# Kernel tuning notes

Measured on AMD Instinct MI355X. Metric: run time of the kernel, lower is better.

The kernel has to match this reference:

```python
import jax, jax.numpy as jnp
import numpy as np

B, N, IN_DIM, L = 4, 512, 256, 128


def setup_inputs() -> dict:
    key = jax.random.key(0)
    k1, k2, k3, k4 = jax.random.split(key, 4)
    x = jax.random.normal(k1, (B, N, IN_DIM), dtype=jnp.float32)
    adj = jnp.ones((B, N, N), dtype=jnp.float32)
    box_num = jax.random.randint(k2, (B, 1), 0, N)  # (B,1) int
    # learned params
    W = jax.random.normal(k3, (L, IN_DIM), dtype=jnp.float32) * 0.05  # projection (no bias)
    a = jax.random.uniform(k4, (L,), dtype=jnp.float32)  # adjacency vector, U(0,1)
    return {"x": x, "adj": adj, "box_num": box_num, "W": W, "a": a}


def reference(x, adj, box_num, W, a):
    Bn, Nn, _ = x.shape
    x_hat = jnp.einsum('bnd,ld->bnl', x, W)  # (B,N,L)
    # dynamic mask: -1 where either node is padding, 0 otherwise (B,N,N)
    valid = jnp.arange(Nn)[None, :] < box_num  # (B,N) bool
    pair = valid[:, None, :] & valid[:, :, None]  # (B,N,N)
    mask = jnp.where(pair, 0.0, -1.0).astype(x.dtype)
    # (|x_i - x_j| + mask) . a  ==  |x_i - x_j| . a  +  mask * sum(a)
    diff = jnp.abs(x_hat[:, :, None, :] - x_hat[:, None, :, :])  # (B,N,N,L) big intermediate
    dist = jnp.einsum('bijd,d->bij', diff, a) + mask * jnp.sum(a)
    out = jax.nn.leaky_relu(dist)  # negative_slope 0.01 matches torch default
    out = out - jnp.max(out, axis=-1, keepdims=True)
    soft = adj * jnp.exp(out)
    soft = soft / jnp.sum(soft, axis=-1, keepdims=True) + 1e-10
    return soft
```

## Files before the change

### kernel.cpp

```cpp
#include <hip/hip_runtime.h>
#include <math.h>

namespace {

constexpr int B_ = 4;
constexpr int N_ = 512;
constexpr int D_ = 256;
constexpr int L_ = 128;
constexpr int TI = 4;

__global__ __launch_bounds__(128) void proj_kernel(
    const float* __restrict__ x, const float* __restrict__ W,
    const float* __restrict__ a, float* __restrict__ xs) {
  const int tid = threadIdx.x;
  const int b = blockIdx.z;
  const int n = blockIdx.y * 128 + tid;
  const int l0 = blockIdx.x * 4;
  const float4* __restrict__ x4 =
      reinterpret_cast<const float4*>(x + (size_t)(b * N_ + n) * D_);
  const float4* __restrict__ W4 = reinterpret_cast<const float4*>(W);
  float acc0 = 0.f, acc1 = 0.f, acc2 = 0.f, acc3 = 0.f;
#pragma unroll 4
  for (int d4 = 0; d4 < D_ / 4; ++d4) {
    const float4 xv = x4[d4];
    const float4 w0 = W4[(l0 + 0) * (D_ / 4) + d4];
    const float4 w1 = W4[(l0 + 1) * (D_ / 4) + d4];
    const float4 w2 = W4[(l0 + 2) * (D_ / 4) + d4];
    const float4 w3 = W4[(l0 + 3) * (D_ / 4) + d4];
    acc0 += xv.x * w0.x + xv.y * w0.y + xv.z * w0.z + xv.w * w0.w;
    acc1 += xv.x * w1.x + xv.y * w1.y + xv.z * w1.z + xv.w * w1.w;
    acc2 += xv.x * w2.x + xv.y * w2.y + xv.z * w2.z + xv.w * w2.w;
    acc3 += xv.x * w3.x + xv.y * w3.y + xv.z * w3.z + xv.w * w3.w;
  }
  float* o = xs + (size_t)(b * L_ + l0) * N_ + n;
  o[0 * N_] = acc0 * a[l0 + 0];
  o[1 * N_] = acc1 * a[l0 + 1];
  o[2 * N_] = acc2 * a[l0 + 2];
  o[3 * N_] = acc3 * a[l0 + 3];
}

__global__ __launch_bounds__(512) void dist_softmax_kernel(
    const float* __restrict__ xs, const float* __restrict__ adj,
    const int* __restrict__ box_num, const float* __restrict__ a,
    float* __restrict__ out) {
  const int t = threadIdx.x;
  const int j = t;
  const int i0 = blockIdx.x * TI;
  const int b = blockIdx.y;
  const int bn = box_num[b];
  const float* __restrict__ xs_b = xs + (size_t)b * L_ * N_;

  __shared__ float xi_l[L_ * TI];
  __shared__ float red[8][TI];
  __shared__ float sa_l[2];
  __shared__ float rmax_s[TI];
  __shared__ float rsinv_s[TI];

  xi_l[t] = xs_b[(t >> 2) * N_ + i0 + (t & 3)];

  {
    float sa = (t < L_) ? a[t] : 0.f;
#pragma unroll
    for (int off = 1; off < 64; off <<= 1) sa += __shfl_xor(sa, off);
    if (t == 0) sa_l[0] = sa;
    if (t == 64) sa_l[1] = sa;
  }
  __syncthreads();
  const float sum_a = sa_l[0] + sa_l[1];

  float acc[TI];
#pragma unroll
  for (int r = 0; r < TI; ++r) acc[r] = 0.f;

  const float4* __restrict__ xi4 = reinterpret_cast<const float4*>(xi_l);
#pragma unroll 4
  for (int l = 0; l < L_; ++l) {
    const float xj = xs_b[l * N_ + j];
    const float4 xi = xi4[l];
    acc[0] += fabsf(xi.x - xj);
    acc[1] += fabsf(xi.y - xj);
    acc[2] += fabsf(xi.z - xj);
    acc[3] += fabsf(xi.w - xj);
  }

  const bool vj = j < bn;
  float val[TI];
#pragma unroll
  for (int r = 0; r < TI; ++r) {
    const bool vi = (i0 + r) < bn;
    const float d = acc[r] - ((vi && vj) ? 0.f : sum_a);
    val[r] = d >= 0.f ? d : 0.01f * d;
  }

  const int lane = t & 63;
  const int wid = t >> 6;

  {
    float wm[TI];
#pragma unroll
    for (int r = 0; r < TI; ++r) {
      float m = val[r];
#pragma unroll
      for (int off = 1; off < 64; off <<= 1) m = fmaxf(m, __shfl_xor(m, off));
      wm[r] = m;
    }
    if (lane == 0) {
#pragma unroll
      for (int r = 0; r < TI; ++r) red[wid][r] = wm[r];
    }
  }
  __syncthreads();
  if (t < TI) {
    float m = red[0][t];
#pragma unroll
    for (int w = 1; w < 8; ++w) m = fmaxf(m, red[w][t]);
    rmax_s[t] = m;
  }
  __syncthreads();

  float e[TI];
  const float* __restrict__ adjp = adj + ((size_t)(b * N_ + i0)) * N_ + j;
#pragma unroll
  for (int r = 0; r < TI; ++r) {
    e[r] = adjp[(size_t)r * N_] * expf(val[r] - rmax_s[r]);
  }

  {
    float wsum[TI];
#pragma unroll
    for (int r = 0; r < TI; ++r) {
      float s = e[r];
#pragma unroll
      for (int off = 1; off < 64; off <<= 1) s += __shfl_xor(s, off);
      wsum[r] = s;
    }
    if (lane == 0) {
#pragma unroll
      for (int r = 0; r < TI; ++r) red[wid][r] = wsum[r];
    }
  }
  __syncthreads();
  if (t < TI) {
    float s = red[0][t];
#pragma unroll
    for (int w = 1; w < 8; ++w) s += red[w][t];
    rsinv_s[t] = 1.0f / s;
  }
  __syncthreads();

  float* __restrict__ op = out + ((size_t)(b * N_ + i0)) * N_ + j;
#pragma unroll
  for (int r = 0; r < TI; ++r) {
    op[(size_t)r * N_] = e[r] * rsinv_s[r] + 1e-10f;
  }
}

}

extern "C" void kernel_launch(void* const* d_in, const int* in_sizes, int n_in,
                              void* d_out, int out_size, void* d_ws,
                              size_t ws_size, hipStream_t stream) {
  const float* x = (const float*)d_in[0];
  const float* adj = (const float*)d_in[1];
  const int* box_num = (const int*)d_in[2];
  const float* W = (const float*)d_in[3];
  const float* a = (const float*)d_in[4];
  float* out = (float*)d_out;
  float* xs = (float*)d_ws;

  dim3 g1(L_ / 4, N_ / 128, B_);
  proj_kernel<<<g1, 128, 0, stream>>>(x, W, a, xs);

  dim3 g2(N_ / TI, B_);
  dist_softmax_kernel<<<g2, 512, 0, stream>>>(xs, adj, box_num, a, out);
}
```

Baseline: 29.87 us.

## Stage x tiles in LDS for projection and double rows per softmax block

```diff
diff --git a/kernel.cpp b/kernel.cpp
--- a/kernel.cpp
+++ b/kernel.cpp
@@ -7,36 +7,64 @@
 constexpr int N_ = 512;
 constexpr int D_ = 256;
 constexpr int L_ = 128;
-constexpr int TI = 4;
-
-__global__ __launch_bounds__(128) void proj_kernel(
+constexpr int TI = 8;
+constexpr int PN = 64;
+constexpr int PL = 16;
+constexpr int PD = 64;
+constexpr int LDSW = 76;
+
+__global__ __launch_bounds__(256) void proj_kernel(
     const float* __restrict__ x, const float* __restrict__ W,
     const float* __restrict__ a, float* __restrict__ xs) {
-  const int tid = threadIdx.x;
+  const int t = threadIdx.x;
   const int b = blockIdx.z;
-  const int n = blockIdx.y * 128 + tid;
-  const int l0 = blockIdx.x * 4;
-  const float4* __restrict__ x4 =
-      reinterpret_cast<const float4*>(x + (size_t)(b * N_ + n) * D_);
-  const float4* __restrict__ W4 = reinterpret_cast<const float4*>(W);
-  float acc0 = 0.f, acc1 = 0.f, acc2 = 0.f, acc3 = 0.f;
-#pragma unroll 4
-  for (int d4 = 0; d4 < D_ / 4; ++d4) {
-    const float4 xv = x4[d4];
-    const float4 w0 = W4[(l0 + 0) * (D_ / 4) + d4];
-    const float4 w1 = W4[(l0 + 1) * (D_ / 4) + d4];
-    const float4 w2 = W4[(l0 + 2) * (D_ / 4) + d4];
-    const float4 w3 = W4[(l0 + 3) * (D_ / 4) + d4];
-    acc0 += xv.x * w0.x + xv.y * w0.y + xv.z * w0.z + xv.w * w0.w;
-    acc1 += xv.x * w1.x + xv.y * w1.y + xv.z * w1.z + xv.w * w1.w;
-    acc2 += xv.x * w2.x + xv.y * w2.y + xv.z * w2.z + xv.w * w2.w;
-    acc3 += xv.x * w3.x + xv.y * w3.y + xv.z * w3.z + xv.w * w3.w;
-  }
-  float* o = xs + (size_t)(b * L_ + l0) * N_ + n;
-  o[0 * N_] = acc0 * a[l0 + 0];
-  o[1 * N_] = acc1 * a[l0 + 1];
-  o[2 * N_] = acc2 * a[l0 + 2];
-  o[3 * N_] = acc3 * a[l0 + 3];
+  const int n0 = blockIdx.y * PN;
+  const int l0 = blockIdx.x * PL;
+
+  __shared__ float xlds[PN * LDSW];
+
+  const int n = t & 63;
+  const int lq = __builtin_amdgcn_readfirstlane(t >> 6);
+  const int lbase = l0 + lq * 4;
+
+  const int sr = t >> 2;
+  const int sc = t & 3;
+
+  float acc[4] = {0.f, 0.f, 0.f, 0.f};
+  const float4* __restrict__ Wb = reinterpret_cast<const float4*>(W);
+
+#pragma unroll
+  for (int ch = 0; ch < D_ / PD; ++ch) {
+    const int d0 = ch * PD;
+    __syncthreads();
+    {
+      const float4* __restrict__ src = reinterpret_cast<const float4*>(
+          x + ((size_t)(b * N_ + n0 + sr)) * D_ + d0);
+      float4* dst = reinterpret_cast<float4*>(xlds + sr * LDSW);
+#pragma unroll
+      for (int i2 = 0; i2 < 4; ++i2) {
+        dst[i2 * 4 + sc] = src[i2 * 4 + sc];
+      }
+    }
+    __syncthreads();
+    const float4* __restrict__ xrow =
+        reinterpret_cast<const float4*>(xlds + n * LDSW);
+#pragma unroll
+    for (int d4 = 0; d4 < PD / 4; ++d4) {
+      const float4 xv = xrow[d4];
+#pragma unroll
+      for (int k = 0; k < 4; ++k) {
+        const float4 wv = Wb[(size_t)(lbase + k) * (D_ / 4) + d0 / 4 + d4];
+        acc[k] += xv.x * wv.x + xv.y * wv.y + xv.z * wv.z + xv.w * wv.w;
+      }
+    }
+  }
+
+#pragma unroll
+  for (int k = 0; k < 4; ++k) {
+    const int l = lbase + k;
+    xs[((size_t)(b * L_ + l)) * N_ + n0 + n] = acc[k] * a[l];
+  }
 }
 
 __global__ __launch_bounds__(512) void dist_softmax_kernel(
@@ -56,7 +84,11 @@
   __shared__ float rmax_s[TI];
   __shared__ float rsinv_s[TI];
 
-  xi_l[t] = xs_b[(t >> 2) * N_ + i0 + (t & 3)];
+#pragma unroll
+  for (int s = 0; s < 2; ++s) {
+    const int idx = t + s * 512;
+    xi_l[idx] = xs_b[(idx >> 3) * N_ + i0 + (idx & 7)];
+  }
 
   {
     float sa = (t < L_) ? a[t] : 0.f;
@@ -76,11 +108,16 @@
 #pragma unroll 4
   for (int l = 0; l < L_; ++l) {
     const float xj = xs_b[l * N_ + j];
-    const float4 xi = xi4[l];
-    acc[0] += fabsf(xi.x - xj);
-    acc[1] += fabsf(xi.y - xj);
-    acc[2] += fabsf(xi.z - xj);
-    acc[3] += fabsf(xi.w - xj);
+    const float4 xiA = xi4[2 * l];
+    const float4 xiB = xi4[2 * l + 1];
+    acc[0] += fabsf(xiA.x - xj);
+    acc[1] += fabsf(xiA.y - xj);
+    acc[2] += fabsf(xiA.z - xj);
+    acc[3] += fabsf(xiA.w - xj);
+    acc[4] += fabsf(xiB.x - xj);
+    acc[5] += fabsf(xiB.y - xj);
+    acc[6] += fabsf(xiB.z - xj);
+    acc[7] += fabsf(xiB.w - xj);
   }
 
   const bool vj = j < bn;
@@ -168,8 +205,8 @@
   float* out = (float*)d_out;
   float* xs = (float*)d_ws;
 
-  dim3 g1(L_ / 4, N_ / 128, B_);
-  proj_kernel<<<g1, 128, 0, stream>>>(x, W, a, xs);
+  dim3 g1(L_ / PL, N_ / PN, B_);
+  proj_kernel<<<g1, 256, 0, stream>>>(x, W, a, xs);
 
   dim3 g2(N_ / TI, B_);
   dist_softmax_kernel<<<g2, 512, 0, stream>>>(xs, adj, box_num, a, out);
```

Result: slower. 31.52 us (+5.5%).
